# Performance work log

Hardware: AMD Instinct MI355X
Metric: run time of the kernel (lower is better)

The kernel has to match this reference:

```python
import jax, jax.numpy as jnp
import numpy as np

# Model dims (Mamba2-2.7B-like)
B_SZ = 1; SEQ = 2048; HID = 2048
INTER = 4096; N_STATE = 128; N_GROUPS = 1; NH = 64; HD = 64
K_CONV = 4; CHUNK = 256
GN = N_GROUPS * N_STATE            # 128
CONV_DIM = INTER + 2 * GN          # 4352
D_IN = 2 * INTER + 2 * GN + NH     # 8512
EPS = 1e-5


def setup_inputs() -> dict:
    key = jax.random.key(0)
    ks = jax.random.split(key, 8)
    return {
        "hidden_states": jax.random.normal(ks[0], (B_SZ, SEQ, HID), jnp.float32),
        "W_in": jax.random.normal(ks[1], (HID, D_IN), jnp.float32) * 0.02,
        "conv_w": jax.random.normal(ks[2], (CONV_DIM, K_CONV), jnp.float32) * 0.2,
        "conv_b": jax.random.normal(ks[3], (CONV_DIM,), jnp.float32) * 0.1,
        "dt_bias": jax.random.uniform(ks[4], (NH,), jnp.float32, -4.0, 0.0),
        "A": -jnp.exp(jax.random.uniform(ks[5], (NH,), jnp.float32, -1.0, 1.0)),
        "D": jnp.ones((NH,), jnp.float32),
        "norm_weight": jnp.ones((INTER,), jnp.float32),
        "W_out": jax.random.normal(ks[6], (INTER, HID), jnp.float32) * 0.02,
    }


def reference(hidden_states, W_in, conv_w, conv_b, dt_bias, A, D, norm_weight, W_out):
    b, S, _ = hidden_states.shape
    # in_proj and split: gate [inter], x/B/C [conv_dim], dt [num_heads]
    proj = hidden_states @ W_in
    gate, xBC, dt = jnp.split(proj, [INTER, INTER + CONV_DIM], axis=-1)
    dt = jax.nn.softplus(dt + dt_bias)  # [b,S,NH]

    # causal depthwise conv1d + SiLU (kernel K, left-padded)
    xp = jnp.pad(xBC, ((0, 0), (K_CONV - 1, 0), (0, 0)))
    conv = conv_b
    for k in range(K_CONV):  # tiny fixed loop over kernel taps
        conv = conv + conv_w[:, k] * xp[:, k:k + S, :]
    xBC = jax.nn.silu(conv)

    x, Bm, Cm = jnp.split(xBC, [INTER, INTER + GN], axis=-1)
    L = CHUNK; nc = S // L
    x_c = x.reshape(b, nc, L, NH, HD)
    rep = NH // N_GROUPS
    B_c = jnp.repeat(Bm.reshape(b, nc, L, N_GROUPS, N_STATE), rep, axis=3)  # bclhn
    C_c = jnp.repeat(Cm.reshape(b, nc, L, N_GROUPS, N_STATE), rep, axis=3)
    dt_c = dt.reshape(b, nc, L, NH)

    dA = dt_c * A                      # [b,c,l,h]  (A < 0)
    cA = jnp.cumsum(dA, axis=2)        # within-chunk cumulative log-decay
    cAt = jnp.transpose(cA, (0, 1, 3, 2))  # [b,c,h,l]

    # intra-chunk: causal decay matrix, (C B^T) masked, weighted by dt
    diff = cAt[..., :, None] - cAt[..., None, :]          # [b,c,h,l,s]
    tril = jnp.tril(jnp.ones((L, L), bool))
    Lmat = jnp.exp(jnp.where(tril, diff, -jnp.inf))
    CB = jnp.einsum('bclhn,bcshn->bchls', C_c, B_c)
    M = CB * Lmat * jnp.transpose(dt_c, (0, 1, 3, 2))[:, :, :, None, :]
    Y_intra = jnp.einsum('bchls,bcshp->bclhp', M, x_c)

    # per-chunk end state contributions
    decay_states = jnp.exp(cA[:, :, -1:, :] - cA)          # [b,c,l,h]
    states = jnp.einsum('bclh,bclhn,bclhp->bchpn', decay_states * dt_c, B_c, x_c)
    chunk_decay = jnp.exp(cA[:, :, -1, :])                 # [b,c,h]

    def step(carry, inp):
        d, st = inp
        new = carry * d[..., None, None] + st
        return new, carry  # emit state entering the chunk

    _, prev = jax.lax.scan(step, jnp.zeros((b, NH, HD, N_STATE), states.dtype),
                           (jnp.moveaxis(chunk_decay, 1, 0), jnp.moveaxis(states, 1, 0)))
    prev = jnp.moveaxis(prev, 0, 1)                        # [b,c,h,p,n]

    Y_inter = jnp.einsum('bclhn,bclh,bchpn->bclhp', C_c, jnp.exp(cA), prev)
    Y = Y_intra + Y_inter + x_c * D[:, None]               # skip D*x per head

    y = Y.reshape(b, S, INTER)
    # gated RMSNorm in fp32
    z = y.astype(jnp.float32) * jax.nn.silu(gate.astype(jnp.float32))
    var = jnp.mean(z * z, axis=-1, keepdims=True)
    z = z * jax.lax.rsqrt(var + EPS) * norm_weight
    return z @ W_out
```

## Files before the change

kernel.cpp:

```cpp
#include <hip/hip_runtime.h>

typedef __bf16 bf16_t;
typedef bf16_t bf16x8 __attribute__((ext_vector_type(8)));
typedef float f32x4 __attribute__((ext_vector_type(4)));
typedef unsigned short u16;
typedef u16 u16x8 __attribute__((ext_vector_type(8)));
typedef u16 u16x4 __attribute__((ext_vector_type(4)));

#define SEQ   2048
#define HID   2048
#define INTER 4096
#define NH    64
#define HD    64
#define CONVD 4352
#define DIN   8512
#define CHNK  256
#define NC    8

__device__ __forceinline__ u16 f2bf(float f) {
  union { float f; unsigned u; } a; a.f = f;
  return (u16)((a.u + 0x7fffu + ((a.u >> 16) & 1u)) >> 16);
}
__device__ __forceinline__ float bf2f(u16 u) {
  union { unsigned u; float f; } a; a.u = ((unsigned)u) << 16;
  return a.f;
}

__device__ __forceinline__ void gl2lds16(const void* g, void* l) {
  auto gp = reinterpret_cast<__attribute__((address_space(1))) void*>(
      (unsigned long long)g);
  auto lp = reinterpret_cast<__attribute__((address_space(3))) void*>(
      (unsigned)(unsigned long long)l);
  __builtin_amdgcn_global_load_lds(gp, lp, 16, 0, 0);
}

__device__ __forceinline__ bf16x8 ds128(unsigned addr) {
  bf16x8 r;
  asm volatile("ds_read_b128 %0, %1" : "=v"(r) : "v"(addr));
  return r;
}

__global__ __launch_bounds__(256) void cvt_bf16(const float* __restrict__ s,
                                                u16* __restrict__ d, int n4) {
  int i = blockIdx.x * 256 + threadIdx.x;
  if (i < n4) {
    f32x4 v = ((const f32x4*)s)[i];
    u16x4 r;
#pragma unroll
    for (int k = 0; k < 4; ++k) r[k] = f2bf(v[k]);
    ((u16x4*)d)[i] = r;
  }
}

__global__ __launch_bounds__(256) void transpose_bf16(const float* __restrict__ src,
                                                      u16* __restrict__ dst,
                                                      int R, int Cc) {
  __shared__ u16 t[64][72];
  const int n0 = blockIdx.x * 64, k0 = blockIdx.y * 64;
  const int tx = threadIdx.x & 15;
  const int ty = threadIdx.x >> 4;
  if (n0 + 63 < Cc) {
#pragma unroll
    for (int j = 0; j < 4; ++j) {
      int k = ty + j * 16;
      f32x4 v = *(const f32x4*)(src + (long)(k0 + k) * Cc + n0 + tx * 4);
#pragma unroll
      for (int e = 0; e < 4; ++e) t[tx * 4 + e][k] = f2bf(v[e]);
    }
  } else {
#pragma unroll
    for (int j = 0; j < 4; ++j) {
      int k = ty + j * 16;
#pragma unroll
      for (int e = 0; e < 4; ++e) {
        int n = n0 + tx * 4 + e;
        t[tx * 4 + e][k] = (n < Cc) ? f2bf(src[(long)(k0 + k) * Cc + n]) : (u16)0;
      }
    }
  }
  __syncthreads();
  const int cg = threadIdx.x & 7;
  const int r0 = threadIdx.x >> 3;
#pragma unroll
  for (int j = 0; j < 2; ++j) {
    int row = r0 + j * 32;
    u16x8 o;
#pragma unroll
    for (int e = 0; e < 8; ++e) o[e] = t[row][cg * 8 + e];
    *(u16x8*)(dst + (long)(n0 + row) * R + k0 + cg * 8) = o;
  }
}

__global__ __launch_bounds__(256, 2) void gemm_bt(const u16* __restrict__ A,
                                                  const u16* __restrict__ Bt,
                                                  float* __restrict__ C,
                                                  int N, int lda, int Klen,
                                                  long zstride) {
  __shared__ __align__(16) u16 As[128 * 64];
  __shared__ __align__(16) u16 Bs[128 * 64];
  const int kz = blockIdx.z;
  A  += (long)kz * Klen;
  Bt += (long)kz * Klen;
  C  += (long)kz * zstride;
  const int nb = gridDim.x * gridDim.y;
  const int id = blockIdx.x + gridDim.x * blockIdx.y;
  const int s = (id & 7) * (nb >> 3) + (id >> 3);
  const long bm = s & 15;
  const long bn = s >> 4;

  const int tid = threadIdx.x;
  const int lane = tid & 63;
  const int w = tid >> 6;
  const int wm = w >> 1, wn = w & 1;

  f32x4 acc[4][4];
#pragma unroll
  for (int i = 0; i < 4; ++i)
#pragma unroll
    for (int j = 0; j < 4; ++j) acc[i][j] = (f32x4){0.f, 0.f, 0.f, 0.f};

  const int srr = lane >> 3;
  const int sc8 = ((lane & 7) ^ srr) * 8;
  const u16* Agw = A + (bm * 128 + w * 8 + srr) * (long)lda + sc8;
  const u16* Bgw = Bt + (bn * 128 + w * 8 + srr) * (long)lda + sc8;
  u16* ldA = As + w * 512 + lane * 8;
  u16* ldB = Bs + w * 512 + lane * 8;
  const int fr = lane & 15, q = lane >> 4;
  const int fx = (fr & 7) << 3;

  for (int k0 = 0; k0 < Klen; k0 += 64) {
    __syncthreads();
#pragma unroll
    for (int t = 0; t < 4; ++t) {
      gl2lds16(Agw + k0 + (long)t * 32 * lda, ldA + t * 2048);
      gl2lds16(Bgw + k0 + (long)t * 32 * lda, ldB + t * 2048);
    }
    __builtin_amdgcn_s_waitcnt(0);
    __syncthreads();
#pragma unroll
    for (int ks = 0; ks < 2; ++ks) {
      bf16x8 af[4], bfv[4];
#pragma unroll
      for (int i = 0; i < 4; ++i)
        af[i] = *(const bf16x8*)(As + ((wm * 64 + i * 16 + fr) << 6) +
                                 ((((ks << 2) + q) << 3) ^ fx));
#pragma unroll
      for (int j = 0; j < 4; ++j)
        bfv[j] = *(const bf16x8*)(Bs + ((wn * 64 + j * 16 + fr) << 6) +
                                  ((((ks << 2) + q) << 3) ^ fx));
#pragma unroll
      for (int i = 0; i < 4; ++i)
#pragma unroll
        for (int j = 0; j < 4; ++j)
          acc[i][j] = __builtin_amdgcn_mfma_f32_16x16x32_bf16(af[i], bfv[j], acc[i][j], 0, 0, 0);
    }
  }
  const int cr = (lane >> 4) * 4;
  const int cc = lane & 15;
#pragma unroll
  for (int i = 0; i < 4; ++i)
#pragma unroll
    for (int j = 0; j < 4; ++j) {
      long r = bm * 128 + wm * 64 + i * 16 + cr;
      long cidx = bn * 128 + wn * 64 + j * 16 + cc;
      float* cp = C + r * (long)N + cidx;
#pragma unroll
      for (int t = 0; t < 4; ++t) cp[(long)t * N] = acc[i][j][t];
    }
}

#define MFMA16(ACC, AF, BF)                                                    \
  _Pragma("unroll") for (int i_ = 0; i_ < 4; ++i_)                             \
  _Pragma("unroll") for (int j_ = 0; j_ < 2; ++j_) {                           \
    ACC[i_][j_] = __builtin_amdgcn_mfma_f32_16x16x32_bf16(                     \
        AF[i_][0], BF[j_][0], ACC[i_][j_], 0, 0, 0);                           \
    ACC[i_][j_] = __builtin_amdgcn_mfma_f32_16x16x32_bf16(                     \
        AF[i_][1], BF[j_][1], ACC[i_][j_], 0, 0, 0);                           \
  }

#define LDAF(DST, SLOT)                                                        \
  {                                                                            \
    unsigned ab_ = (unsigned)(unsigned long long)(&Abuf[SLOT][0]);             \
    _Pragma("unroll") for (int i_ = 0; i_ < 4; ++i_) {                         \
      unsigned ro_ = ab_ + (((wm * 64 + i_ * 16 + fr) << 6) << 1);             \
      DST[i_][0] = ds128(ro_ + (ke0 << 1));                                    \
      DST[i_][1] = ds128(ro_ + (ke1 << 1));                                    \
    }                                                                          \
  }

#define LDBF(DST, SLOT)                                                        \
  {                                                                            \
    unsigned bb_ = (unsigned)(unsigned long long)(&Bbuf[SLOT][0]);             \
    _Pragma("unroll") for (int j_ = 0; j_ < 2; ++j_) {                         \
      unsigned ro_ = bb_ + (((wn * 32 + j_ * 16 + fr) << 6) << 1);             \
      DST[j_][0] = ds128(ro_ + (ke0 << 1));                                    \
      DST[j_][1] = ds128(ro_ + (ke1 << 1));                                    \
    }                                                                          \
  }

#define STAGE(G, HO, KO, SLOT, BUF)                                            \
  {                                                                            \
    const u16* g_ = (G) + (HO) + (KO);                                         \
    gl2lds16(g_ + off1, BUF[SLOT] + lo1);                                      \
    gl2lds16(g_ + off2, BUF[SLOT] + lo2);                                      \
  }

#define PH_FENCE()                                                             \
  asm volatile("s_waitcnt lgkmcnt(0)" ::: "memory");                           \
  __builtin_amdgcn_sched_barrier(0);

template <int BFOUT>
__global__ __launch_bounds__(512, 2) void gemm256(const u16* __restrict__ A,
                                                  const u16* __restrict__ Bt,
                                                  void* __restrict__ Cv,
                                                  int N, int lda, int Klen,
                                                  long zstride) {
  __shared__ __align__(16) u16 Abuf[4][128 * 64];
  __shared__ __align__(16) u16 Bbuf[4][128 * 64];

  const int kz = blockIdx.z;
  A  += (long)kz * Klen;
  Bt += (long)kz * Klen;
  const long czoff = (long)kz * zstride;

  const int nb = gridDim.x * gridDim.y;
  const int id = blockIdx.x + gridDim.x * blockIdx.y;
  const int s = (id & 7) * (nb >> 3) + (id >> 3);
  const long bm = s & 7;
  const long bn = s >> 3;

  const int tid = threadIdx.x;
  const int lane = tid & 63;
  const int w = tid >> 6;
  const int wm = w >> 2;
  const int wn = w & 3;
  const int fr = lane & 15, q = lane >> 4;
  const int ke0 = (q ^ (fr & 7)) << 3;
  const int ke1 = ((4 + q) ^ (fr & 7)) << 3;

  const int sr1 = (w << 4) + (lane >> 3);
  const int sr2 = sr1 + 8;
  const int kcp = lane & 7;
  const long off1 = (long)sr1 * lda + ((kcp ^ (sr1 & 7)) << 3);
  const long off2 = (long)sr2 * lda + ((kcp ^ (sr2 & 7)) << 3);
  const int lo1 = (w << 10) + (lane << 3);
  const int lo2 = lo1 + 512;
  const long h128 = 128L * lda;

  const u16* gA = A + bm * 256 * lda;
  const u16* gB = Bt + bn * 256 * lda;

  f32x4 acc00[4][2], acc01[4][2], acc10[4][2], acc11[4][2];
#pragma unroll
  for (int i = 0; i < 4; ++i)
#pragma unroll
    for (int j = 0; j < 2; ++j) {
      acc00[i][j] = (f32x4){0.f, 0.f, 0.f, 0.f};
      acc01[i][j] = (f32x4){0.f, 0.f, 0.f, 0.f};
      acc10[i][j] = (f32x4){0.f, 0.f, 0.f, 0.f};
      acc11[i][j] = (f32x4){0.f, 0.f, 0.f, 0.f};
    }

  const int NT = Klen >> 6;

  STAGE(gA, 0L, 0L, 0, Abuf);
  STAGE(gB, 0L, 0L, 0, Bbuf);
  STAGE(gB, h128, 0L, 1, Bbuf);
  STAGE(gA, h128, 0L, 1, Abuf);
  STAGE(gA, 0L, 64L, 2, Abuf);
  STAGE(gB, 0L, 64L, 2, Bbuf);
  STAGE(gB, h128, 64L, 3, Bbuf);
  STAGE(gA, h128, 64L, 3, Abuf);
  asm volatile("s_waitcnt vmcnt(8)" ::: "memory");
  __builtin_amdgcn_s_barrier();

  for (int T = 0; T < NT; ++T) {
    const int t2 = (T << 1) & 3;
    const int t2p1 = (t2 + 1) & 3;
    const long kT2 = (long)(T + 2) << 6;
    const bool g2 = (T + 2 < NT);
    bf16x8 a0[4][2], a1[4][2], b0[2][2], b1[2][2];

    LDAF(a0, t2);
    LDBF(b0, t2);
    asm volatile("s_waitcnt lgkmcnt(8)" ::: "memory");
    __builtin_amdgcn_s_barrier();
    PH_FENCE();
    __builtin_amdgcn_s_setprio(1);
    MFMA16(acc00, a0, b0);
    __builtin_amdgcn_s_setprio(0);
    __builtin_amdgcn_s_barrier();

    LDBF(b1, t2p1);
    if (g2) STAGE(gA, 0L, kT2, t2, Abuf);
    __builtin_amdgcn_s_barrier();
    PH_FENCE();
    __builtin_amdgcn_s_setprio(1);
    MFMA16(acc01, a0, b1);
    __builtin_amdgcn_s_setprio(0);
    __builtin_amdgcn_s_barrier();

    LDAF(a1, t2p1);
    if (g2) STAGE(gB, 0L, kT2, t2, Bbuf);
    __builtin_amdgcn_s_barrier();
    PH_FENCE();
    __builtin_amdgcn_s_setprio(1);
    MFMA16(acc10, a1, b0);
    __builtin_amdgcn_s_setprio(0);
    __builtin_amdgcn_s_barrier();

    if (g2) {
      STAGE(gB, h128, kT2, t2p1, Bbuf);
      STAGE(gA, h128, kT2, t2p1, Abuf);
    }
    __builtin_amdgcn_s_barrier();
    PH_FENCE();
    __builtin_amdgcn_s_setprio(1);
    MFMA16(acc11, a1, b1);
    __builtin_amdgcn_s_setprio(0);
    if (g2)
      asm volatile("s_waitcnt vmcnt(8)" ::: "memory");
    else
      asm volatile("s_waitcnt vmcnt(0)" ::: "memory");
    __builtin_amdgcn_s_barrier();
  }

  const int cr = (lane >> 4) << 2;
  const int cc = lane & 15;
  const long r0 = bm * 256 + wm * 64 + cr;
  const long c0 = bn * 256 + wn * 32 + cc;
#define CWRITE(ACC, QA, QB)                                                    \
  _Pragma("unroll") for (int i_ = 0; i_ < 4; ++i_)                             \
  _Pragma("unroll") for (int j_ = 0; j_ < 2; ++j_) {                           \
    long r_ = r0 + (QA)*128 + i_ * 16;                                         \
    long c_ = c0 + (QB)*128 + j_ * 16;                                         \
    if (c_ < N) {                                                              \
      long base_ = czoff + r_ * (long)N + c_;                                  \
      _Pragma("unroll") for (int t_ = 0; t_ < 4; ++t_) {                       \
        if (BFOUT)                                                             \
          ((u16*)Cv)[base_ + (long)t_ * N] = f2bf(ACC[i_][j_][t_]);            \
        else                                                                   \
          ((float*)Cv)[base_ + (long)t_ * N] = ACC[i_][j_][t_];                \
      }                                                                        \
    }                                                                          \
  }
  CWRITE(acc00, 0, 0)
  CWRITE(acc01, 0, 1)
  CWRITE(acc10, 1, 0)
  CWRITE(acc11, 1, 1)
#undef CWRITE
}

__global__ __launch_bounds__(256) void add4_kernel(const float* __restrict__ a,
                                                   float* __restrict__ o) {
  int i = blockIdx.x * 256 + threadIdx.x;
  f32x4 r = ((const f32x4*)a)[i];
  r += ((const f32x4*)(a + 4194304L))[i];
  r += ((const f32x4*)(a + 8388608L))[i];
  r += ((const f32x4*)(a + 12582912L))[i];
  ((f32x4*)o)[i] = r;
}

__global__ __launch_bounds__(256) void conv_silu_t(const u16* __restrict__ pb,
                                                   const float* __restrict__ Cs,
                                                   const float* __restrict__ cw,
                                                   const float* __restrict__ cb,
                                                   u16* __restrict__ xbf,
                                                   u16* __restrict__ xT) {
  __shared__ float ld[35][33];
  __shared__ u16 tt[32][34];
  const int c0 = blockIdx.x * 32, t0 = blockIdx.y * 32;
  const int tx = threadIdx.x & 31, ty = threadIdx.x >> 5;
  const bool mainreg = (c0 < 4096);
  for (int i = ty; i < 35; i += 8) {
    int t = t0 - 3 + i;
    float v = 0.f;
    if (t >= 0) {
      if (mainreg) {
        v = bf2f(pb[(long)t * 8192 + 4096 + c0 + tx]);
      } else {
        long idx = (long)t * 384 + (c0 - 4096) + tx;
        v = Cs[idx];
        v += Cs[idx + 786432L];
        v += Cs[idx + 1572864L];
        v += Cs[idx + 2359296L];
      }
    }
    ld[i][tx] = v;
  }
  const int c = c0 + tx;
  const float w0 = cw[c * 4 + 0], w1 = cw[c * 4 + 1], w2 = cw[c * 4 + 2],
              w3 = cw[c * 4 + 3], bias = cb[c];
  __syncthreads();
  for (int i = ty; i < 32; i += 8) {
    float a = bias + w0 * ld[i][tx] + w1 * ld[i + 1][tx] + w2 * ld[i + 2][tx] +
              w3 * ld[i + 3][tx];
    u16 v = f2bf(a / (1.f + __expf(-a)));
    xbf[(long)(t0 + i) * CONVD + c] = v;
    tt[i][tx] = v;
  }
  __syncthreads();
  if (c0 < 4224) {
    for (int i = ty; i < 32; i += 8)
      xT[(long)(c0 + i) * 2048 + t0 + tx] = tt[tx][i];
  }
}

__global__ __launch_bounds__(256) void dt_cumsum(const float* __restrict__ Cs,
                                                 const float* __restrict__ dtb,
                                                 const float* __restrict__ A,
                                                 float* __restrict__ dt2,
                                                 float* __restrict__ cA2) {
  __shared__ float sc[256];
  int c = blockIdx.x, h = blockIdx.y, l = threadIdx.x;
  long idx = (long)(c * 256 + l) * 384 + 256 + h;
  float v = Cs[idx];
  v += Cs[idx + 786432L];
  v += Cs[idx + 1572864L];
  v += Cs[idx + 2359296L];
  v += dtb[h];
  float sp = (v > 20.f) ? v : log1pf(__expf(v));
  dt2[h * 2048 + c * 256 + l] = sp;
  sc[l] = sp * A[h];
  __syncthreads();
  for (int off = 1; off < 256; off <<= 1) {
    float t = (l >= off) ? sc[l - off] : 0.f;
    __syncthreads();
    sc[l] += t;
    __syncthreads();
  }
  cA2[h * 2048 + c * 256 + l] = sc[l];
}

__global__ __launch_bounds__(256, 2) void cb_gemm(const u16* __restrict__ xbf,
                                                  float* __restrict__ CB) {
  __shared__ __align__(16) u16 As[128 * 32];
  __shared__ __align__(16) u16 Bs[128 * 32];
  const int tid = threadIdx.x;
  const int lane = tid & 63;
  const int w = tid >> 6;
  const int wm = w >> 1, wn = w & 1;
  const int bm = blockIdx.y, bn = blockIdx.x, c = blockIdx.z;

  f32x4 acc[4][4];
#pragma unroll
  for (int i = 0; i < 4; ++i)
#pragma unroll
    for (int j = 0; j < 4; ++j) acc[i][j] = (f32x4){0.f, 0.f, 0.f, 0.f};

  const int sr = w * 32 + (lane >> 2);
  const int sc = ((lane & 3) ^ ((lane >> 2) & 3)) * 8;
  const u16* Ag = xbf + (long)(c * 256 + bm * 128) * CONVD + 4224;
  const u16* Bg = xbf + (long)(c * 256 + bn * 128) * CONVD + 4096;
  u16* lA0 = As + w * 1024 + lane * 8;
  u16* lA1 = As + w * 1024 + 512 + lane * 8;
  u16* lB0 = Bs + w * 1024 + lane * 8;
  u16* lB1 = Bs + w * 1024 + 512 + lane * 8;
  const int fr = lane & 15, q = lane >> 4;
  const int pc = ((q ^ (fr & 3)) << 3);

  for (int k0 = 0; k0 < 128; k0 += 32) {
    __syncthreads();
    const u16* a0 = Ag + (long)sr * CONVD + k0 + sc;
    const u16* b0 = Bg + (long)sr * CONVD + k0 + sc;
    gl2lds16(a0, lA0);
    gl2lds16(a0 + 16L * CONVD, lA1);
    gl2lds16(b0, lB0);
    gl2lds16(b0 + 16L * CONVD, lB1);
    __builtin_amdgcn_s_waitcnt(0);
    __syncthreads();
    bf16x8 af[4], bfv[4];
#pragma unroll
    for (int i = 0; i < 4; ++i)
      af[i] = *(const bf16x8*)(As + ((wm * 64 + i * 16 + fr) << 5) + pc);
#pragma unroll
    for (int j = 0; j < 4; ++j)
      bfv[j] = *(const bf16x8*)(Bs + ((wn * 64 + j * 16 + fr) << 5) + pc);
#pragma unroll
    for (int i = 0; i < 4; ++i)
#pragma unroll
      for (int j = 0; j < 4; ++j)
        acc[i][j] = __builtin_amdgcn_mfma_f32_16x16x32_bf16(af[i], bfv[j], acc[i][j], 0, 0, 0);
  }
  const int cr = (lane >> 4) * 4;
  const int cc = lane & 15;
  float* Cc = CB + (long)c * 65536;
#pragma unroll
  for (int i = 0; i < 4; ++i)
#pragma unroll
    for (int j = 0; j < 4; ++j) {
      int r = bm * 128 + wm * 64 + i * 16 + cr;
      int cidx = bn * 128 + wn * 64 + j * 16 + cc;
      float* cp = Cc + (long)r * 256 + cidx;
#pragma unroll
      for (int t = 0; t < 4; ++t) cp[t * 256] = acc[i][j][t];
    }
}

#define LDM 72
__global__ __launch_bounds__(256) void states_kernel(const u16* __restrict__ xT,
                                                     const float* __restrict__ dt2,
                                                     const float* __restrict__ cA2,
                                                     float* __restrict__ stT) {
  __shared__ __align__(16) u16 Ms[128 * LDM];
  __shared__ __align__(16) u16 Xs[64 * LDM];
  __shared__ float wl[256];
  const int c = blockIdx.x, h = blockIdx.y;
  const int tid = threadIdx.x;
  const int lane = tid & 63, w = tid >> 6;
  const int fr = lane & 15, q = lane >> 4;
  {
    float calast = cA2[h * 2048 + c * 256 + 255];
    float ca = cA2[h * 2048 + c * 256 + tid];
    wl[tid] = __expf(calast - ca) * dt2[h * 2048 + c * 256 + tid];
  }
  f32x4 acc[2][4];
#pragma unroll
  for (int i = 0; i < 2; ++i)
#pragma unroll
    for (int j = 0; j < 4; ++j) acc[i][j] = (f32x4){0.f, 0.f, 0.f, 0.f};

  const int lc8 = (tid & 7) * 8;
  const int rn = tid >> 3;
  __syncthreads();

  for (int kt = 0; kt < 4; ++kt) {
    __syncthreads();
#pragma unroll
    for (int r = 0; r < 4; ++r) {
      int n = rn + 32 * r;
      u16x8 raw = *(const u16x8*)(xT + (long)(4096 + n) * 2048 + c * 256 + kt * 64 + lc8);
      union { u16 u[8]; bf16x8 v; } pk;
#pragma unroll
      for (int u = 0; u < 8; ++u)
        pk.u[u] = f2bf(bf2f(raw[u]) * wl[kt * 64 + lc8 + u]);
      *(bf16x8*)(Ms + n * LDM + lc8) = pk.v;
    }
#pragma unroll
    for (int r = 0; r < 2; ++r) {
      int p = rn + 32 * r;
      *(bf16x8*)(Xs + p * LDM + lc8) =
          *(const bf16x8*)(xT + (long)(h * 64 + p) * 2048 + c * 256 + kt * 64 + lc8);
    }
    __syncthreads();
#pragma unroll
    for (int ks = 0; ks < 64; ks += 32) {
      bf16x8 af[2], xf[4];
#pragma unroll
      for (int i = 0; i < 2; ++i)
        af[i] = *(const bf16x8*)(Ms + (w * 32 + i * 16 + fr) * LDM + ks + q * 8);
#pragma unroll
      for (int j = 0; j < 4; ++j)
        xf[j] = *(const bf16x8*)(Xs + (j * 16 + fr) * LDM + ks + q * 8);
#pragma unroll
      for (int i = 0; i < 2; ++i)
#pragma unroll
        for (int j = 0; j < 4; ++j)
          acc[i][j] = __builtin_amdgcn_mfma_f32_16x16x32_bf16(af[i], xf[j], acc[i][j], 0, 0, 0);
    }
  }
  const int cr = (lane >> 4) * 4;
  const int cc = lane & 15;
  float* outp = stT + (long)(c * 64 + h) * 8192;
#pragma unroll
  for (int i = 0; i < 2; ++i)
#pragma unroll
    for (int j = 0; j < 4; ++j) {
      int n = w * 32 + i * 16 + cr;
      int p = j * 16 + cc;
#pragma unroll
      for (int t = 0; t < 4; ++t) outp[(n + t) * 64 + p] = acc[i][j][t];
    }
}

__global__ __launch_bounds__(256) void scan_kernel(const float* __restrict__ stT,
                                                   const float* __restrict__ cA2,
                                                   u16* __restrict__ prevT) {
  int id = blockIdx.x * 256 + threadIdx.x;
  int h = id >> 13;
  float acc = 0.f;
#pragma unroll
  for (int c = 0; c < NC; ++c) {
    prevT[(long)c * 524288 + id] = f2bf(acc);
    float cd = __expf(cA2[h * 2048 + c * 256 + 255]);
    acc = acc * cd + stT[(long)c * 524288 + id];
  }
}

__global__ __launch_bounds__(256) void ssm_y_kernel(const u16* __restrict__ xbf,
                                                    const u16* __restrict__ xT,
                                                    const float* __restrict__ dt2,
                                                    const float* __restrict__ cA2,
                                                    const float* __restrict__ CB,
                                                    const u16* __restrict__ prevT,
                                                    const float* __restrict__ Dp,
                                                    u16* __restrict__ Y) {
  __shared__ __align__(16) u16 Ms[256 * LDM];
  __shared__ __align__(16) u16 Xt[64 * LDM];
  __shared__ float cas[256];
  __shared__ float dts[256];
  const int c = blockIdx.x, h = blockIdx.y;
  const int tid = threadIdx.x;
  const int lane = tid & 63;
  const int w = tid >> 6;
  const int fr = lane & 15, q = lane >> 4;

  cas[tid] = cA2[h * 2048 + c * 256 + tid];
  dts[tid] = dt2[h * 2048 + c * 256 + tid];

  f32x4 acc[4][4];
#pragma unroll
  for (int i = 0; i < 4; ++i)
#pragma unroll
    for (int j = 0; j < 4; ++j) acc[i][j] = (f32x4){0.f, 0.f, 0.f, 0.f};

  const int sg = (tid & 7) * 8;
  const int lb = tid >> 3;
  const int xp = tid & 63;
  const int xq = tid >> 6;

  __syncthreads();

  for (int kt = 0; kt < 6; ++kt) {
    __syncthreads();
    if (kt < 4) {
      const int s0 = kt * 64;
      f32x4 e0 = *(const f32x4*)&cas[s0 + sg];
      f32x4 e1 = *(const f32x4*)&cas[s0 + sg + 4];
      f32x4 d0 = *(const f32x4*)&dts[s0 + sg];
      f32x4 d1 = *(const f32x4*)&dts[s0 + sg + 4];
#pragma unroll
      for (int k = 0; k < 8; ++k) {
        const int l = lb + 32 * k;
        const float cal = cas[l];
        const float* cb = CB + (long)c * 65536 + (long)l * 256 + s0 + sg;
        f32x4 c0 = *(const f32x4*)cb;
        f32x4 c1 = *(const f32x4*)(cb + 4);
        union { u16 u[8]; bf16x8 v; } pk;
#pragma unroll
        for (int u = 0; u < 8; ++u) {
          int s = s0 + sg + u;
          float cv = (u < 4) ? c0[u] : c1[u - 4];
          float cs = (u < 4) ? e0[u] : e1[u - 4];
          float dv = (u < 4) ? d0[u] : d1[u - 4];
          float m = (s <= l) ? cv * __expf(cal - cs) * dv : 0.f;
          pk.u[u] = f2bf(m);
        }
        *(bf16x8*)(Ms + l * LDM + sg) = pk.v;
      }
#pragma unroll
      for (int r = 0; r < 2; ++r) {
        int p = (tid >> 3) + 32 * r;
        *(bf16x8*)(Xt + p * LDM + sg) =
            *(const bf16x8*)(xT + (long)(h * 64 + p) * 2048 + c * 256 + s0 + sg);
      }
    } else {
      const int n0 = (kt - 4) * 64;
#pragma unroll
      for (int k = 0; k < 8; ++k) {
        const int l = lb + 32 * k;
        const float ea = __expf(cas[l]);
        u16x8 raw = *(const u16x8*)(xbf + (long)(c * 256 + l) * CONVD + 4224 + n0 + sg);
        union { u16 u[8]; bf16x8 v; } pk;
#pragma unroll
        for (int u = 0; u < 8; ++u) pk.u[u] = f2bf(ea * bf2f(raw[u]));
        *(bf16x8*)(Ms + l * LDM + sg) = pk.v;
      }
      const u16* pT = prevT + (long)(c * 64 + h) * 8192;
#pragma unroll
      for (int half = 0; half < 2; ++half) {
        const int nb2 = xq * 16 + half * 8;
        union { u16 u[8]; bf16x8 v; } pk;
#pragma unroll
        for (int u = 0; u < 8; ++u) pk.u[u] = pT[(n0 + nb2 + u) * 64 + xp];
        *(bf16x8*)(Xt + xp * LDM + nb2) = pk.v;
      }
    }
    __syncthreads();
#pragma unroll
    for (int ks = 0; ks < 64; ks += 32) {
      bf16x8 af[4], bfv[4];
#pragma unroll
      for (int i = 0; i < 4; ++i)
        af[i] = *(const bf16x8*)(Ms + (w * 64 + i * 16 + fr) * LDM + ks + q * 8);
#pragma unroll
      for (int j = 0; j < 4; ++j)
        bfv[j] = *(const bf16x8*)(Xt + (j * 16 + fr) * LDM + ks + q * 8);
#pragma unroll
      for (int i = 0; i < 4; ++i)
#pragma unroll
        for (int j = 0; j < 4; ++j)
          acc[i][j] = __builtin_amdgcn_mfma_f32_16x16x32_bf16(af[i], bfv[j], acc[i][j], 0, 0, 0);
    }
  }

  const int cr = (lane >> 4) * 4;
  const int cc = lane & 15;
  const float dh = Dp[h];
#pragma unroll
  for (int i = 0; i < 4; ++i)
#pragma unroll
    for (int j = 0; j < 4; ++j) {
      const int p = j * 16 + cc;
#pragma unroll
      for (int t = 0; t < 4; ++t) {
        const int row = w * 64 + i * 16 + cr + t;
        const float xv = bf2f(xbf[(long)(c * 256 + row) * CONVD + h * 64 + p]);
        Y[(long)(c * 256 + row) * 4096 + h * 64 + p] = f2bf(acc[i][j][t] + dh * xv);
      }
    }
}

__global__ __launch_bounds__(256) void rmsnorm_kernel(const u16* __restrict__ Y,
                                                      const u16* __restrict__ pb,
                                                      const float* __restrict__ nw,
                                                      u16* __restrict__ zbf) {
  __shared__ float red[256];
  int t = blockIdx.x, tid = threadIdx.x;
  const u16* y = Y + (long)t * 4096;
  const u16* g = pb + (long)t * 8192;
  float zv[16];
  float s = 0.f;
#pragma unroll
  for (int k = 0; k < 16; ++k) {
    int i = tid + k * 256;
    float gv = bf2f(g[i]);
    float z = bf2f(y[i]) * (gv / (1.f + __expf(-gv)));
    zv[k] = z;
    s += z * z;
  }
  red[tid] = s;
  __syncthreads();
  if (tid < 128) red[tid] += red[tid + 128];
  __syncthreads();
  if (tid < 64) {
    float v = red[tid] + red[tid + 64];
    v += __shfl_down(v, 32);
    v += __shfl_down(v, 16);
    v += __shfl_down(v, 8);
    v += __shfl_down(v, 4);
    v += __shfl_down(v, 2);
    v += __shfl_down(v, 1);
    if (tid == 0) red[0] = v;
  }
  __syncthreads();
  float scale = rsqrtf(red[0] * (1.f / 4096.f) + 1e-5f);
#pragma unroll
  for (int k = 0; k < 16; ++k) {
    int i = tid + k * 256;
    zbf[(long)t * 4096 + i] = f2bf(zv[k] * scale * nw[i]);
  }
}

extern "C" void kernel_launch(void* const* d_in, const int* in_sizes, int n_in,
                              void* d_out, int out_size, void* d_ws, size_t ws_size,
                              hipStream_t stream) {
  const float* hidden = (const float*)d_in[0];
  const float* Win    = (const float*)d_in[1];
  const float* convw  = (const float*)d_in[2];
  const float* convb  = (const float*)d_in[3];
  const float* dtb    = (const float*)d_in[4];
  const float* Ap     = (const float*)d_in[5];
  const float* Dp     = (const float*)d_in[6];
  const float* nw     = (const float*)d_in[7];
  const float* Wout   = (const float*)d_in[8];
  float* out = (float*)d_out;
  char* ws = (char*)d_ws;

  u16*   hb    = (u16*)(ws + 0);
  u16*   WinT  = (u16*)(ws + 8388608L);
  u16*   pb    = (u16*)(ws + 43515904L);
  u16*   WoutT = (u16*)(ws + 113770496L);
  u16*   xbf   = (u16*)(ws + 130547712L);
  u16*   xT    = (u16*)(ws + 148373504L);
  float* dt2   = (float*)(ws + 165675008L);
  float* cA2   = (float*)(ws + 166199296L);
  float* CBv   = (float*)(ws + 166723584L);
  float* stT   = (float*)(ws + 168820736L);
  u16*   prevT = (u16*)(ws + 185597952L);
  u16*   zbf   = (u16*)(ws + 202375168L);
  u16*   Y     = (u16*)(ws + 0);
  float* Cp    = (float*)(ws + 43515904L);
  float* Cs    = (float*)(ws + 168820736L);

  cvt_bf16<<<4096, 256, 0, stream>>>(hidden, hb, 1048576);
  transpose_bf16<<<dim3(134, 32), 256, 0, stream>>>(Win, WinT, 2048, 8512);
  transpose_bf16<<<dim3(32, 64), 256, 0, stream>>>(Wout, WoutT, 4096, 2048);
  gemm256<1><<<dim3(32, 8, 1), 512, 0, stream>>>(hb, WinT, pb, 8192, 2048, 2048, 0L);
  gemm_bt<<<dim3(3, 16, 4), 256, 0, stream>>>(hb, WinT + 8192L * 2048, Cs,
                                              384, 2048, 512, 786432L);
  conv_silu_t<<<dim3(136, 64), 256, 0, stream>>>(pb, Cs, convw, convb, xbf, xT);
  dt_cumsum<<<dim3(8, 64), 256, 0, stream>>>(Cs, dtb, Ap, dt2, cA2);
  cb_gemm<<<dim3(2, 2, 8), 256, 0, stream>>>(xbf, CBv);
  states_kernel<<<dim3(8, 64), 256, 0, stream>>>(xT, dt2, cA2, stT);
  scan_kernel<<<2048, 256, 0, stream>>>(stT, cA2, prevT);
  ssm_y_kernel<<<dim3(8, 64), 256, 0, stream>>>(xbf, xT, dt2, cA2, CBv, prevT, Dp, Y);
  rmsnorm_kernel<<<2048, 256, 0, stream>>>(Y, pb, nw, zbf);
  gemm256<0><<<dim3(8, 8, 4), 512, 0, stream>>>(zbf, WoutT, Cp, 2048, 4096, 1024, 4194304L);
  add4_kernel<<<4096, 256, 0, stream>>>(Cp, out);
}
```

Measured before the change: 387.4 us.

## Fuse prep kernels into one launch and vectorize scan and rmsnorm accesses

Merges the hidden-state bf16 conversion and both weight transposes into a single kernel launch that branches on block index, removing two launches. The scan kernel now processes four state elements per thread with 128-bit loads and 64-bit stores, using a quarter of the blocks. RMSNorm loads and stores 16 contiguous elements per thread with vector accesses instead of strided scalar ones. These are small memory-efficiency and launch-overhead changes in mostly cheap kernels. The dominant GEMM and SSM kernels are untouched.

After: 383.8 us. Within noise of the previous version (-0.9%).

```diff
diff --git a/kernel.cpp b/kernel.cpp
--- a/kernel.cpp
+++ b/kernel.cpp
@@ -40,25 +40,35 @@
   return r;
 }
 
-__global__ __launch_bounds__(256) void cvt_bf16(const float* __restrict__ s,
-                                                u16* __restrict__ d, int n4) {
-  int i = blockIdx.x * 256 + threadIdx.x;
-  if (i < n4) {
-    f32x4 v = ((const f32x4*)s)[i];
+__global__ __launch_bounds__(256) void prep_fused(const float* __restrict__ hidden,
+                                                  u16* __restrict__ hb,
+                                                  const float* __restrict__ Win,
+                                                  u16* __restrict__ WinT,
+                                                  const float* __restrict__ Wout,
+                                                  u16* __restrict__ WoutT) {
+  __shared__ u16 t[64][72];
+  const int b = blockIdx.x, tid = threadIdx.x;
+  if (b < 4096) {
+    int i = b * 256 + tid;
+    f32x4 v = ((const f32x4*)hidden)[i];
     u16x4 r;
 #pragma unroll
     for (int k = 0; k < 4; ++k) r[k] = f2bf(v[k]);
-    ((u16x4*)d)[i] = r;
-  }
-}
-
-__global__ __launch_bounds__(256) void transpose_bf16(const float* __restrict__ src,
-                                                      u16* __restrict__ dst,
-                                                      int R, int Cc) {
-  __shared__ u16 t[64][72];
-  const int n0 = blockIdx.x * 64, k0 = blockIdx.y * 64;
-  const int tx = threadIdx.x & 15;
-  const int ty = threadIdx.x >> 4;
+    ((u16x4*)hb)[i] = r;
+    return;
+  }
+  const float* src; u16* dst; int R, Cc, n0, k0;
+  if (b < 8384) {
+    int idx = b - 4096;
+    src = Win; dst = WinT; R = 2048; Cc = 8512;
+    n0 = (idx % 134) * 64; k0 = (idx / 134) * 64;
+  } else {
+    int idx = b - 8384;
+    src = Wout; dst = WoutT; R = 4096; Cc = 2048;
+    n0 = (idx % 32) * 64; k0 = (idx / 32) * 64;
+  }
+  const int tx = tid & 15;
+  const int ty = tid >> 4;
   if (n0 + 63 < Cc) {
 #pragma unroll
     for (int j = 0; j < 4; ++j) {
@@ -79,8 +89,8 @@
     }
   }
   __syncthreads();
-  const int cg = threadIdx.x & 7;
-  const int r0 = threadIdx.x >> 3;
+  const int cg = tid & 7;
+  const int r0 = tid >> 3;
 #pragma unroll
   for (int j = 0; j < 2; ++j) {
     int row = r0 + j * 32;
@@ -576,14 +586,18 @@
 __global__ __launch_bounds__(256) void scan_kernel(const float* __restrict__ stT,
                                                    const float* __restrict__ cA2,
                                                    u16* __restrict__ prevT) {
-  int id = blockIdx.x * 256 + threadIdx.x;
-  int h = id >> 13;
-  float acc = 0.f;
+  int g = blockIdx.x * 256 + threadIdx.x;
+  int h = g >> 11;
+  f32x4 acc = (f32x4){0.f, 0.f, 0.f, 0.f};
 #pragma unroll
   for (int c = 0; c < NC; ++c) {
-    prevT[(long)c * 524288 + id] = f2bf(acc);
+    u16x4 o;
+#pragma unroll
+    for (int e = 0; e < 4; ++e) o[e] = f2bf(acc[e]);
+    ((u16x4*)(prevT + (long)c * 524288))[g] = o;
     float cd = __expf(cA2[h * 2048 + c * 256 + 255]);
-    acc = acc * cd + stT[(long)c * 524288 + id];
+    f32x4 st = ((const f32x4*)(stT + (long)c * 524288))[g];
+    acc = acc * cd + st;
   }
 }
 
@@ -717,16 +731,26 @@
                                                       u16* __restrict__ zbf) {
   __shared__ float red[256];
   int t = blockIdx.x, tid = threadIdx.x;
-  const u16* y = Y + (long)t * 4096;
-  const u16* g = pb + (long)t * 8192;
+  const u16* y = Y + (long)t * 4096 + tid * 16;
+  const u16* g = pb + (long)t * 8192 + tid * 16;
+  u16x8 yv0 = *(const u16x8*)y;
+  u16x8 yv1 = *(const u16x8*)(y + 8);
+  u16x8 gv0 = *(const u16x8*)g;
+  u16x8 gv1 = *(const u16x8*)(g + 8);
   float zv[16];
   float s = 0.f;
 #pragma unroll
-  for (int k = 0; k < 16; ++k) {
-    int i = tid + k * 256;
-    float gv = bf2f(g[i]);
-    float z = bf2f(y[i]) * (gv / (1.f + __expf(-gv)));
-    zv[k] = z;
+  for (int e = 0; e < 8; ++e) {
+    float gv = bf2f(gv0[e]);
+    float z = bf2f(yv0[e]) * (gv / (1.f + __expf(-gv)));
+    zv[e] = z;
+    s += z * z;
+  }
+#pragma unroll
+  for (int e = 0; e < 8; ++e) {
+    float gv = bf2f(gv1[e]);
+    float z = bf2f(yv1[e]) * (gv / (1.f + __expf(-gv)));
+    zv[8 + e] = z;
     s += z * z;
   }
   red[tid] = s;
@@ -745,11 +769,20 @@
   }
   __syncthreads();
   float scale = rsqrtf(red[0] * (1.f / 4096.f) + 1e-5f);
-#pragma unroll
-  for (int k = 0; k < 16; ++k) {
-    int i = tid + k * 256;
-    zbf[(long)t * 4096 + i] = f2bf(zv[k] * scale * nw[i]);
-  }
+  const float* wp = nw + tid * 16;
+  f32x4 w0 = ((const f32x4*)wp)[0], w1 = ((const f32x4*)wp)[1];
+  f32x4 w2 = ((const f32x4*)wp)[2], w3 = ((const f32x4*)wp)[3];
+  u16x8 o0, o1;
+#pragma unroll
+  for (int e = 0; e < 4; ++e) {
+    o0[e]     = f2bf(zv[e]      * scale * w0[e]);
+    o0[4 + e] = f2bf(zv[4 + e]  * scale * w1[e]);
+    o1[e]     = f2bf(zv[8 + e]  * scale * w2[e]);
+    o1[4 + e] = f2bf(zv[12 + e] * scale * w3[e]);
+  }
+  u16* zp = zbf + (long)t * 4096 + tid * 16;
+  *(u16x8*)zp = o0;
+  *(u16x8*)(zp + 8) = o1;
 }
 
 extern "C" void kernel_launch(void* const* d_in, const int* in_sizes, int n_in,
@@ -783,9 +816,7 @@
   float* Cp    = (float*)(ws + 43515904L);
   float* Cs    = (float*)(ws + 168820736L);
 
-  cvt_bf16<<<4096, 256, 0, stream>>>(hidden, hb, 1048576);
-  transpose_bf16<<<dim3(134, 32), 256, 0, stream>>>(Win, WinT, 2048, 8512);
-  transpose_bf16<<<dim3(32, 64), 256, 0, stream>>>(Wout, WoutT, 4096, 2048);
+  prep_fused<<<10432, 256, 0, stream>>>(hidden, hb, Win, WinT, Wout, WoutT);
   gemm256<1><<<dim3(32, 8, 1), 512, 0, stream>>>(hb, WinT, pb, 8192, 2048, 2048, 0L);
   gemm_bt<<<dim3(3, 16, 4), 256, 0, stream>>>(hb, WinT + 8192L * 2048, Cs,
                                               384, 2048, 512, 786432L);
@@ -793,7 +824,7 @@
   dt_cumsum<<<dim3(8, 64), 256, 0, stream>>>(Cs, dtb, Ap, dt2, cA2);
   cb_gemm<<<dim3(2, 2, 8), 256, 0, stream>>>(xbf, CBv);
   states_kernel<<<dim3(8, 64), 256, 0, stream>>>(xT, dt2, cA2, stT);
-  scan_kernel<<<2048, 256, 0, stream>>>(stT, cA2, prevT);
+  scan_kernel<<<512, 256, 0, stream>>>(stT, cA2, prevT);
   ssm_y_kernel<<<dim3(8, 64), 256, 0, stream>>>(xbf, xT, dt2, cA2, CBv, prevT, Dp, Y);
   rmsnorm_kernel<<<2048, 256, 0, stream>>>(Y, pb, nw, zbf);
   gemm256<0><<<dim3(8, 8, 4), 512, 0, stream>>>(zbf, WoutT, Cp, 2048, 4096, 1024, 4194304L);
```
